# Kernel optimization log

Hardware: AMD Instinct MI355X
Metric: run time of the kernel (lower is better)

The kernel has to match this reference:

```python
import jax, jax.numpy as jnp
import numpy as np

WINDOW = (6, 7, 7)  # (agent_size, window_size, window_size)
HEADS = 8           # dim // dim_head = 256 // 32


def _relative_position_index(ws):
    d, h, w = ws
    coords = np.stack(np.meshgrid(np.arange(d), np.arange(h), np.arange(w), indexing='ij'))
    cf = coords.reshape(3, -1)                      # [3, n]
    rel = cf[:, :, None] - cf[:, None, :]           # [3, n, n]
    rel = rel.transpose(1, 2, 0).copy()             # [n, n, 3]
    rel[..., 0] += d - 1
    rel[..., 1] += h - 1
    rel[..., 2] += w - 1
    rel[..., 0] *= (2 * h - 1) * (2 * w - 1)
    rel[..., 1] *= (2 * w - 1)
    return rel.sum(-1)                              # [n, n] int

REL_IDX = jnp.asarray(_relative_position_index(WINDOW))


def setup_inputs() -> dict:
    key = jax.random.key(0)
    ks = jax.random.split(key, 7)
    dim = 256
    n_bias = (2 * WINDOW[0] - 1) * (2 * WINDOW[1] - 1) * (2 * WINDOW[2] - 1)  # 1859
    s = 0.02
    return {
        'x': jax.random.normal(ks[0], (2, 6, 12, 12, 7, 7, dim), jnp.float32),
        'Wq': jax.random.normal(ks[1], (dim, dim), jnp.float32) * s,
        'bq': jax.random.normal(ks[2], (dim,), jnp.float32) * s,
        'Wkv': jax.random.normal(ks[3], (dim, 2 * dim), jnp.float32) * s,
        'bkv': jax.random.normal(ks[4], (2 * dim,), jnp.float32) * s,
        'Wout': jax.random.normal(ks[5], (dim, dim), jnp.float32) * s,
        'bias_table': jax.random.normal(ks[6], (n_bias, HEADS), jnp.float32) * s,
    }


def reference(x, Wq, bq, Wkv, bkv, Wout, bias_table):
    b, l, gx, gy, w1, w2, d = x.shape
    h = HEADS
    dh = d // h
    n = l * w1 * w2
    B = b * gx * gy
    # 'b l x y w1 w2 d -> (b x y) (l w1 w2) d'  (agent-major token order)
    xt = jnp.transpose(x, (0, 2, 3, 1, 4, 5, 6)).reshape(B, n, d)
    q = xt @ Wq + bq                                  # [B, n, d]
    kv = xt @ Wkv + bkv                               # [B, n, 2d]
    k, v = kv[..., :d], kv[..., d:]
    split = lambda t: t.reshape(B, n, h, dh).transpose(0, 2, 1, 3)  # [B, h, n, dh]
    q, k, v = split(q), split(k), split(v)
    scale = dh ** -0.5
    sim = jnp.einsum('bhid,bhjd->bhij', q * scale, k)  # [B, h, n, n]
    bias = bias_table[REL_IDX]                         # [n, n, h]
    sim = sim + jnp.transpose(bias, (2, 0, 1))[None]
    attn = jax.nn.softmax(sim, axis=-1)
    out = jnp.einsum('bhij,bhjd->bhid', attn, v)       # [B, h, n, dh]
    out = out.transpose(0, 2, 1, 3).reshape(B, n, d) @ Wout
    # '(b x y) (l w1 w2) d -> b l x y w1 w2 d'
    out = out.reshape(b, gx, gy, l, w1, w2, d)
    return jnp.transpose(out, (0, 3, 1, 2, 4, 5, 6))
```

## Files before the change

### kernel.cpp

```cpp
#include <hip/hip_runtime.h>

#define DIM    256
#define NWIN   294
#define BWIN   288
#define MROWS  (BWIN * NWIN)
#define MPAD   84736
#define NHEADS 8
#define DH     32
#define NBIAS  1859

typedef __attribute__((ext_vector_type(8))) short  short8;
typedef __attribute__((ext_vector_type(4))) float  f32x4;

__device__ __forceinline__ unsigned short f2bf(float f) {
    unsigned int u = __float_as_uint(f);
    u += 0x7FFFu + ((u >> 16) & 1u);
    return (unsigned short)(u >> 16);
}

__device__ __forceinline__ void gl_lds16(const void* g, void* l) {
    __builtin_amdgcn_global_load_lds((const __attribute__((address_space(1))) unsigned int*)g,
                                     (__attribute__((address_space(3))) unsigned int*)l,
                                     16, 0, 0);
}

__global__ __launch_bounds__(256) void prep_x(const float* __restrict__ x,
                                              unsigned short* __restrict__ Xb)
{
    const int g   = blockIdx.x * 256 + threadIdx.x;
    const int row = g >> 5;
    const int col = (g & 31) * 8;
    if (row >= MPAD) return;
    uint4 pk;
    if (row < MROWS) {
        const int bw = row / NWIN, rw = row - bw * NWIN;
        const int bb = bw / 144,  r2 = bw - bb * 144;
        const int gxi = r2 / 12,  gyi = r2 - gxi * 12;
        const int lz = rw / 49,   r3 = rw - lz * 49;
        const int wa = r3 / 7,    wb = r3 - wa * 7;
        const float* src = x + ((((((size_t)bb * 6 + lz) * 12 + gxi) * 12 + gyi) * 7 + wa) * 7 + wb) * DIM + col;
        const float4 f0 = *(const float4*)(src);
        const float4 f1 = *(const float4*)(src + 4);
        pk.x = (unsigned)f2bf(f0.x) | ((unsigned)f2bf(f0.y) << 16);
        pk.y = (unsigned)f2bf(f0.z) | ((unsigned)f2bf(f0.w) << 16);
        pk.z = (unsigned)f2bf(f1.x) | ((unsigned)f2bf(f1.y) << 16);
        pk.w = (unsigned)f2bf(f1.z) | ((unsigned)f2bf(f1.w) << 16);
    } else {
        pk = (uint4){0u, 0u, 0u, 0u};
    }
    *(uint4*)(Xb + (size_t)row * 256 + col) = pk;
}

__global__ __launch_bounds__(256) void prep_w(const float* __restrict__ Wq,
                                              const float* __restrict__ Wkv,
                                              const float* __restrict__ Wout,
                                              unsigned short* __restrict__ Wt,
                                              unsigned short* __restrict__ Wot)
{
    const int g = blockIdx.x * 256 + threadIdx.x;
    if (g < 768 * 256) {
        const int n = g >> 8, k = g & 255;
        const float v = (n < 256) ? Wq[k * 256 + n] : Wkv[k * 512 + (n - 256)];
        Wt[g] = f2bf(v);
    } else {
        const int g2 = g - 768 * 256;
        const int n = g2 >> 8, k = g2 & 255;
        Wot[g2] = f2bf(Wout[k * 256 + n]);
    }
}

__global__ __launch_bounds__(256) void gemm_qkv(
    const unsigned short* __restrict__ Xb, const unsigned short* __restrict__ Wt,
    const float* __restrict__ bq, const float* __restrict__ bkv,
    unsigned short* __restrict__ Qb, unsigned short* __restrict__ Kb,
    unsigned short* __restrict__ Vtb)
{
    __shared__ __align__(16) unsigned short As[128 * 64];
    __shared__ __align__(16) unsigned short Bs[128 * 64];

    const int bn = blockIdx.x % 6;
    const int bm = blockIdx.x / 6;
    const int tileM = bm * 128;
    const int tileN = bn * 128;

    const int t    = threadIdx.x;
    const int w    = t >> 6;
    const int lane = t & 63;
    const int quad = lane >> 4;
    const int l15  = lane & 15;
    const int wm   = w >> 1, wn = w & 1;

    const int rA = lane >> 3;
    const int kA = (lane & 7) * 8;
    const unsigned short* aBase = Xb + ((size_t)tileM + rA) * 256 + kA;
    const unsigned short* bBase = Wt + ((size_t)tileN + rA) * 256 + kA;

    f32x4 acc[4][4] = {};

    for (int kb = 0; kb < 4; ++kb) {
        const int k0 = kb * 64;
        __syncthreads();
#pragma unroll
        for (int i = 0; i < 4; ++i) {
            const int c = w * 4 + i;
            gl_lds16(aBase + (size_t)c * 8 * 256 + k0, &As[c * 512]);
            gl_lds16(bBase + (size_t)c * 8 * 256 + k0, &Bs[c * 512]);
        }
        __syncthreads();
#pragma unroll
        for (int c2 = 0; c2 < 2; ++c2) {
            const int kk = c2 * 32 + quad * 8;
            short8 a[4], b[4];
#pragma unroll
            for (int mi = 0; mi < 4; ++mi)
                a[mi] = *(const short8*)&As[(wm * 64 + mi * 16 + l15) * 64 + kk];
#pragma unroll
            for (int ni = 0; ni < 4; ++ni)
                b[ni] = *(const short8*)&Bs[(wn * 64 + ni * 16 + l15) * 64 + kk];
#pragma unroll
            for (int mi = 0; mi < 4; ++mi)
#pragma unroll
                for (int ni = 0; ni < 4; ++ni)
                    acc[mi][ni] = __builtin_amdgcn_mfma_f32_16x16x32_bf16(a[mi], b[ni], acc[mi][ni], 0, 0, 0);
        }
    }

    const int colB = tileN + wn * 64;
    float bias[4];
#pragma unroll
    for (int ni = 0; ni < 4; ++ni) {
        const int n = colB + ni * 16 + l15;
        bias[ni] = (n < 256) ? bq[n] : bkv[n - 256];
    }
    const int rowB = tileM + wm * 64 + quad * 4;
#pragma unroll
    for (int mi = 0; mi < 4; ++mi) {
#pragma unroll
        for (int r = 0; r < 4; ++r) {
            const int row = rowB + mi * 16 + r;
            if (row < MROWS) {
                const int bw = row / NWIN;
                const int rw = row - bw * NWIN;
#pragma unroll
                for (int ni = 0; ni < 4; ++ni) {
                    const int n = colB + ni * 16 + l15;
                    const unsigned short v = f2bf(acc[mi][ni][r] + bias[ni]);
                    const int ch = n & 255;
                    const int hd = ch >> 5, di = ch & 31;
                    if (n < 512) {
                        unsigned short* dst = (n < 256) ? Qb : Kb;
                        dst[((size_t)(bw * NHEADS + hd) * NWIN + rw) * DH + di] = v;
                    } else {
                        Vtb[((size_t)(bw * NHEADS + hd) * DH + di) * NWIN + rw] = v;
                    }
                }
            }
        }
    }
}

__global__ __launch_bounds__(256, 3) void attn_kernel(
    const unsigned short* __restrict__ Qb, const unsigned short* __restrict__ Kb,
    const unsigned short* __restrict__ Vtb, const float* __restrict__ bias_table,
    unsigned short* __restrict__ Ob)
{
    const int bh   = blockIdx.x;
    const int bwin = bh >> 3;
    const int h    = bh & 7;

    __shared__ __align__(16) unsigned short Ks[304 * 32];
    __shared__ __align__(16) unsigned short Vts[32 * 328];
    __shared__ __align__(16) unsigned short Pc[4 * 16 * 32];
    __shared__ float          biasH[NBIAS];
    __shared__ unsigned short cIdx[304];

    const int t    = threadIdx.x;
    const int w    = t >> 6;
    const int lane = t & 63;
    const int quad = lane >> 4;
    const int l15  = lane & 15;

    {
        const uint4* Kg4 = (const uint4*)(Kb + (size_t)bh * (NWIN * DH));
        for (int i = t; i < (NWIN * DH) / 8; i += 256) ((uint4*)Ks)[i] = Kg4[i];
        for (int i = NWIN * DH + t; i < 304 * 32; i += 256) Ks[i] = 0;
    }
    {
        const unsigned short* Vg = Vtb + (size_t)bh * (DH * NWIN);
        for (int i = t; i < 32 * 328; i += 256) {
            const int r = i / 328, c = i - r * 328;
            Vts[i] = (c < NWIN) ? Vg[r * NWIN + c] : (unsigned short)0;
        }
    }
    for (int i = t; i < NBIAS; i += 256) biasH[i] = bias_table[i * NHEADS + h];
    for (int i = t; i < 304; i += 256) {
        if (i < NWIN) {
            const int l = i / 49, r = i - l * 49;
            cIdx[i] = (unsigned short)(169 * l + 13 * (r / 7) + (r - (r / 7) * 7));
        } else cIdx[i] = 0;
    }
    __syncthreads();

    const float scale = 0.17677669529663687f;
    const unsigned short* Qg = Qb + (size_t)bh * (NWIN * DH);
    unsigned short* Pw = Pc + w * (16 * 32);

#pragma unroll
    for (int r5 = 0; r5 < 5; ++r5) {
        const int it = 4 * r5 + w;
        if (it < 19) {
            short8 qf;
            const int qrow = it * 16 + l15;
            if (qrow < NWIN) qf = *(const short8*)(Qg + qrow * DH + quad * 8);
            else             qf = (short8){0,0,0,0,0,0,0,0};

            f32x4 S[19];
#pragma unroll
            for (int jt = 0; jt < 19; ++jt) {
                const short8 bf = *(const short8*)(Ks + (jt * 16 + l15) * 32 + quad * 8);
                S[jt] = __builtin_amdgcn_mfma_f32_16x16x32_bf16(qf, bf, (f32x4){0.f,0.f,0.f,0.f}, 0, 0, 0);
            }

            int cj[19];
#pragma unroll
            for (int jt = 0; jt < 19; ++jt) cj[jt] = cIdx[jt * 16 + l15];

            const int rowb = it * 16 + quad * 4;
            float inv[4];
#pragma unroll
            for (int r = 0; r < 4; ++r) {
                const int ci = (int)cIdx[rowb + r] + 929;
                float m = -1e30f;
#pragma unroll
                for (int jt = 0; jt < 19; ++jt) {
                    float s = S[jt][r] * scale + biasH[ci - cj[jt]];
                    if (jt == 18 && l15 >= 6) s = -1e30f;
                    S[jt][r] = s;
                    m = fmaxf(m, s);
                }
                m = fmaxf(m, __shfl_xor(m, 1));
                m = fmaxf(m, __shfl_xor(m, 2));
                m = fmaxf(m, __shfl_xor(m, 4));
                m = fmaxf(m, __shfl_xor(m, 8));
                float lsum = 0.f;
#pragma unroll
                for (int jt = 0; jt < 19; ++jt) {
                    const float p = __expf(S[jt][r] - m);
                    S[jt][r] = p;
                    lsum += p;
                }
                lsum += __shfl_xor(lsum, 1);
                lsum += __shfl_xor(lsum, 2);
                lsum += __shfl_xor(lsum, 4);
                lsum += __shfl_xor(lsum, 8);
                inv[r] = 1.0f / lsum;
            }

            f32x4 o0 = {0.f,0.f,0.f,0.f}, o1 = {0.f,0.f,0.f,0.f};
#pragma unroll
            for (int kt = 0; kt < 10; ++kt) {
                const int jt0 = 2 * kt, jt1 = 2 * kt + 1;
#pragma unroll
                for (int r = 0; r < 4; ++r) {
                    Pw[(quad * 4 + r) * 32 + l15]      = f2bf(S[jt0][r]);
                    Pw[(quad * 4 + r) * 32 + 16 + l15] = (jt1 < 19) ? f2bf(S[jt1][r]) : (unsigned short)0;
                }
                __asm__ volatile("s_waitcnt lgkmcnt(0)" ::: "memory");
                const short8 pa = *(const short8*)(Pw + l15 * 32 + quad * 8);
                const short8 v0 = *(const short8*)(Vts + l15 * 328 + kt * 32 + quad * 8);
                const short8 v1 = *(const short8*)(Vts + (16 + l15) * 328 + kt * 32 + quad * 8);
                o0 = __builtin_amdgcn_mfma_f32_16x16x32_bf16(pa, v0, o0, 0, 0, 0);
                o1 = __builtin_amdgcn_mfma_f32_16x16x32_bf16(pa, v1, o1, 0, 0, 0);
                __asm__ volatile("s_waitcnt lgkmcnt(0)" ::: "memory");
            }

#pragma unroll
            for (int r = 0; r < 4; ++r) {
                const int rg = it * 16 + quad * 4 + r;
                if (rg < NWIN) {
                    unsigned short* op = Ob + ((size_t)bwin * NWIN + rg) * DIM + h * DH;
                    op[l15]      = f2bf(o0[r] * inv[r]);
                    op[16 + l15] = f2bf(o1[r] * inv[r]);
                }
            }
        }
    }
}

__global__ __launch_bounds__(256) void gemm_out(
    const unsigned short* __restrict__ Ob, const unsigned short* __restrict__ Wot,
    float* __restrict__ out)
{
    __shared__ __align__(16) unsigned short As[128 * 64];
    __shared__ __align__(16) unsigned short Bs[128 * 64];

    const int bn = blockIdx.x & 1;
    const int bm = blockIdx.x >> 1;
    const int tileM = bm * 128;
    const int tileN = bn * 128;

    const int t    = threadIdx.x;
    const int w    = t >> 6;
    const int lane = t & 63;
    const int quad = lane >> 4;
    const int l15  = lane & 15;
    const int wm   = w >> 1, wn = w & 1;

    const int rA = lane >> 3;
    const int kA = (lane & 7) * 8;
    const unsigned short* aBase = Ob  + ((size_t)tileM + rA) * 256 + kA;
    const unsigned short* bBase = Wot + ((size_t)tileN + rA) * 256 + kA;

    f32x4 acc[4][4] = {};

    for (int kb = 0; kb < 4; ++kb) {
        const int k0 = kb * 64;
        __syncthreads();
#pragma unroll
        for (int i = 0; i < 4; ++i) {
            const int c = w * 4 + i;
            gl_lds16(aBase + (size_t)c * 8 * 256 + k0, &As[c * 512]);
            gl_lds16(bBase + (size_t)c * 8 * 256 + k0, &Bs[c * 512]);
        }
        __syncthreads();
#pragma unroll
        for (int c2 = 0; c2 < 2; ++c2) {
            const int kk = c2 * 32 + quad * 8;
            short8 a[4], b[4];
#pragma unroll
            for (int mi = 0; mi < 4; ++mi)
                a[mi] = *(const short8*)&As[(wm * 64 + mi * 16 + l15) * 64 + kk];
#pragma unroll
            for (int ni = 0; ni < 4; ++ni)
                b[ni] = *(const short8*)&Bs[(wn * 64 + ni * 16 + l15) * 64 + kk];
#pragma unroll
            for (int mi = 0; mi < 4; ++mi)
#pragma unroll
                for (int ni = 0; ni < 4; ++ni)
                    acc[mi][ni] = __builtin_amdgcn_mfma_f32_16x16x32_bf16(a[mi], b[ni], acc[mi][ni], 0, 0, 0);
        }
    }

    const int colB = tileN + wn * 64;
    const int rowB = tileM + wm * 64 + quad * 4;
#pragma unroll
    for (int mi = 0; mi < 4; ++mi) {
#pragma unroll
        for (int r = 0; r < 4; ++r) {
            const int row = rowB + mi * 16 + r;
            if (row < MROWS) {
                const int bw = row / NWIN, rw = row - bw * NWIN;
                const int bb = bw / 144,  r2 = bw - bb * 144;
                const int gxi = r2 / 12,  gyi = r2 - gxi * 12;
                const int lz = rw / 49,   r3 = rw - lz * 49;
                const int wa = r3 / 7,    wb = r3 - wa * 7;
                float* orow = out + ((((((size_t)bb * 6 + lz) * 12 + gxi) * 12 + gyi) * 7 + wa) * 7 + wb) * DIM;
#pragma unroll
                for (int ni = 0; ni < 4; ++ni)
                    orow[colB + ni * 16 + l15] = acc[mi][ni][r];
            }
        }
    }
}

extern "C" void kernel_launch(void* const* d_in, const int* in_sizes, int n_in,
                              void* d_out, int out_size, void* d_ws, size_t ws_size,
                              hipStream_t stream)
{
    const float* x          = (const float*)d_in[0];
    const float* Wq         = (const float*)d_in[1];
    const float* bq         = (const float*)d_in[2];
    const float* Wkv        = (const float*)d_in[3];
    const float* bkv        = (const float*)d_in[4];
    const float* Wout       = (const float*)d_in[5];
    const float* bias_table = (const float*)d_in[6];
    float* out = (float*)d_out;

    const size_t planePad = (size_t)MPAD * DIM;
    const size_t plane    = (size_t)MROWS * DIM;
    unsigned short* Xb  = (unsigned short*)d_ws;
    unsigned short* Qb  = Xb + planePad;
    unsigned short* Kb  = Qb + plane;
    unsigned short* Vtb = Kb + plane;
    unsigned short* Ob  = Vtb + plane;
    unsigned short* Wt  = Ob + planePad;
    unsigned short* Wot = Wt + 768 * 256;

    prep_x<<<MPAD / 8, 256, 0, stream>>>(x, Xb);
    prep_w<<<1024, 256, 0, stream>>>(Wq, Wkv, Wout, Wt, Wot);
    gemm_qkv<<<662 * 6, 256, 0, stream>>>(Xb, Wt, bq, bkv, Qb, Kb, Vtb);
    attn_kernel<<<BWIN * NHEADS, 256, 0, stream>>>(Qb, Kb, Vtb, bias_table, Ob);
    gemm_out<<<662 * 2, 256, 0, stream>>>(Ob, Wot, out);
}
```

Measured before the change: 443.8 us.

## Restructure attention softmax: transposed QK, no max, register P shuffle, MFMA row sums

```diff
diff --git a/kernel.cpp b/kernel.cpp
--- a/kernel.cpp
+++ b/kernel.cpp
@@ -1,4 +1,5 @@
 #include <hip/hip_runtime.h>
+#include <hip/hip_bf16.h>
 
 #define DIM    256
 #define NWIN   294
@@ -16,6 +17,13 @@
     unsigned int u = __float_as_uint(f);
     u += 0x7FFFu + ((u >> 16) & 1u);
     return (unsigned short)(u >> 16);
+}
+
+__device__ __forceinline__ unsigned pk2bf(float a, float b) {
+    __hip_bfloat162 h = __float22bfloat162_rn(float2{a, b});
+    unsigned u;
+    __builtin_memcpy(&u, &h, 4);
+    return u;
 }
 
 __device__ __forceinline__ void gl_lds16(const void* g, void* l) {
@@ -41,10 +49,10 @@
         const float* src = x + ((((((size_t)bb * 6 + lz) * 12 + gxi) * 12 + gyi) * 7 + wa) * 7 + wb) * DIM + col;
         const float4 f0 = *(const float4*)(src);
         const float4 f1 = *(const float4*)(src + 4);
-        pk.x = (unsigned)f2bf(f0.x) | ((unsigned)f2bf(f0.y) << 16);
-        pk.y = (unsigned)f2bf(f0.z) | ((unsigned)f2bf(f0.w) << 16);
-        pk.z = (unsigned)f2bf(f1.x) | ((unsigned)f2bf(f1.y) << 16);
-        pk.w = (unsigned)f2bf(f1.z) | ((unsigned)f2bf(f1.w) << 16);
+        pk.x = pk2bf(f0.x, f0.y);
+        pk.y = pk2bf(f0.z, f0.w);
+        pk.z = pk2bf(f1.x, f1.y);
+        pk.w = pk2bf(f1.z, f1.w);
     } else {
         pk = (uint4){0u, 0u, 0u, 0u};
     }
@@ -168,11 +176,10 @@
     const int bwin = bh >> 3;
     const int h    = bh & 7;
 
-    __shared__ __align__(16) unsigned short Ks[304 * 32];
+    __shared__ __align__(16) unsigned short Ks[304 * 40];
     __shared__ __align__(16) unsigned short Vts[32 * 328];
-    __shared__ __align__(16) unsigned short Pc[4 * 16 * 32];
-    __shared__ float          biasH[NBIAS];
-    __shared__ unsigned short cIdx[304];
+    __shared__ float          biasHs[NBIAS];
+    __shared__ __align__(8) unsigned short cIdx[304];
 
     const int t    = threadIdx.x;
     const int w    = t >> 6;
@@ -181,9 +188,13 @@
     const int l15  = lane & 15;
 
     {
-        const uint4* Kg4 = (const uint4*)(Kb + (size_t)bh * (NWIN * DH));
-        for (int i = t; i < (NWIN * DH) / 8; i += 256) ((uint4*)Ks)[i] = Kg4[i];
-        for (int i = NWIN * DH + t; i < 304 * 32; i += 256) Ks[i] = 0;
+        const unsigned short* Kg = Kb + (size_t)bh * (NWIN * DH);
+        for (int i = t; i < 304 * 4; i += 256) {
+            const int row = i >> 2, seg = i & 3;
+            uint4 v = (uint4){0u, 0u, 0u, 0u};
+            if (row < NWIN) v = *(const uint4*)(Kg + row * 32 + seg * 8);
+            *(uint4*)(Ks + row * 40 + seg * 8) = v;
+        }
     }
     {
         const unsigned short* Vg = Vtb + (size_t)bh * (DH * NWIN);
@@ -192,7 +203,7 @@
             Vts[i] = (c < NWIN) ? Vg[r * NWIN + c] : (unsigned short)0;
         }
     }
-    for (int i = t; i < NBIAS; i += 256) biasH[i] = bias_table[i * NHEADS + h];
+    for (int i = t; i < NBIAS; i += 256) biasHs[i] = bias_table[i * NHEADS + h] * 1.44269504088896f;
     for (int i = t; i < 304; i += 256) {
         if (i < NWIN) {
             const int l = i / 49, r = i - l * 49;
@@ -201,9 +212,11 @@
     }
     __syncthreads();
 
-    const float scale = 0.17677669529663687f;
+    const float SL2E = 0.25503486f;
     const unsigned short* Qg = Qb + (size_t)bh * (NWIN * DH);
-    unsigned short* Pw = Pc + w * (16 * 32);
+    const int   srcB = ((quad & 1) << 5) + l15;
+    const bool  hiSel = (quad >= 2);
+    const short8 ones = (short8){0x3F80,0x3F80,0x3F80,0x3F80,0x3F80,0x3F80,0x3F80,0x3F80};
 
 #pragma unroll
     for (int r5 = 0; r5 < 5; ++r5) {
@@ -214,73 +227,70 @@
             if (qrow < NWIN) qf = *(const short8*)(Qg + qrow * DH + quad * 8);
             else             qf = (short8){0,0,0,0,0,0,0,0};
 
+            const int ciB = (int)cIdx[it * 16 + l15] + 929;
+            const float* bbase = biasHs + ciB;
+
             f32x4 S[19];
 #pragma unroll
             for (int jt = 0; jt < 19; ++jt) {
-                const short8 bf = *(const short8*)(Ks + (jt * 16 + l15) * 32 + quad * 8);
-                S[jt] = __builtin_amdgcn_mfma_f32_16x16x32_bf16(qf, bf, (f32x4){0.f,0.f,0.f,0.f}, 0, 0, 0);
-            }
-
-            int cj[19];
-#pragma unroll
-            for (int jt = 0; jt < 19; ++jt) cj[jt] = cIdx[jt * 16 + l15];
-
-            const int rowb = it * 16 + quad * 4;
-            float inv[4];
-#pragma unroll
-            for (int r = 0; r < 4; ++r) {
-                const int ci = (int)cIdx[rowb + r] + 929;
-                float m = -1e30f;
-#pragma unroll
-                for (int jt = 0; jt < 19; ++jt) {
-                    float s = S[jt][r] * scale + biasH[ci - cj[jt]];
-                    if (jt == 18 && l15 >= 6) s = -1e30f;
-                    S[jt][r] = s;
-                    m = fmaxf(m, s);
+                const short8 kf = *(const short8*)(Ks + (jt * 16 + l15) * 40 + quad * 8);
+                S[jt] = __builtin_amdgcn_mfma_f32_16x16x32_bf16(kf, qf, (f32x4){0.f,0.f,0.f,0.f}, 0, 0, 0);
+            }
+
+            unsigned pk0[20], pk1[20];
+            pk0[19] = 0u; pk1[19] = 0u;
+#pragma unroll
+            for (int jt = 0; jt < 19; ++jt) {
+                const ushort4 c4 = *(const ushort4*)(cIdx + jt * 16 + quad * 4);
+                float p0 = exp2f(fmaf(S[jt][0], SL2E, bbase[-(int)c4.x]));
+                float p1 = exp2f(fmaf(S[jt][1], SL2E, bbase[-(int)c4.y]));
+                float p2 = exp2f(fmaf(S[jt][2], SL2E, bbase[-(int)c4.z]));
+                float p3 = exp2f(fmaf(S[jt][3], SL2E, bbase[-(int)c4.w]));
+                if (jt == 18) {
+                    if (quad * 4 + 0 >= 6) p0 = 0.f;
+                    if (quad * 4 + 1 >= 6) p1 = 0.f;
+                    if (quad * 4 + 2 >= 6) p2 = 0.f;
+                    if (quad * 4 + 3 >= 6) p3 = 0.f;
                 }
-                m = fmaxf(m, __shfl_xor(m, 1));
-                m = fmaxf(m, __shfl_xor(m, 2));
-                m = fmaxf(m, __shfl_xor(m, 4));
-                m = fmaxf(m, __shfl_xor(m, 8));
-                float lsum = 0.f;
-#pragma unroll
-                for (int jt = 0; jt < 19; ++jt) {
-                    const float p = __expf(S[jt][r] - m);
-                    S[jt][r] = p;
-                    lsum += p;
-                }
-                lsum += __shfl_xor(lsum, 1);
-                lsum += __shfl_xor(lsum, 2);
-                lsum += __shfl_xor(lsum, 4);
-                lsum += __shfl_xor(lsum, 8);
-                inv[r] = 1.0f / lsum;
-            }
-
-            f32x4 o0 = {0.f,0.f,0.f,0.f}, o1 = {0.f,0.f,0.f,0.f};
+                pk0[jt] = pk2bf(p0, p1);
+                pk1[jt] = pk2bf(p2, p3);
+            }
+
+            f32x4 o0 = {0.f,0.f,0.f,0.f}, o1 = {0.f,0.f,0.f,0.f}, o2 = {0.f,0.f,0.f,0.f};
 #pragma unroll
             for (int kt = 0; kt < 10; ++kt) {
-                const int jt0 = 2 * kt, jt1 = 2 * kt + 1;
-#pragma unroll
-                for (int r = 0; r < 4; ++r) {
-                    Pw[(quad * 4 + r) * 32 + l15]      = f2bf(S[jt0][r]);
-                    Pw[(quad * 4 + r) * 32 + 16 + l15] = (jt1 < 19) ? f2bf(S[jt1][r]) : (unsigned short)0;
-                }
-                __asm__ volatile("s_waitcnt lgkmcnt(0)" ::: "memory");
-                const short8 pa = *(const short8*)(Pw + l15 * 32 + quad * 8);
+                const int e0 = (int)pk0[2 * kt], e1 = (int)pk0[2 * kt + 1];
+                const int f0 = (int)pk1[2 * kt], f1 = (int)pk1[2 * kt + 1];
+                const unsigned aLo = (unsigned)__shfl(e0, srcB);
+                const unsigned aHi = (unsigned)__shfl(e1, srcB);
+                const unsigned bLo = (unsigned)__shfl(f0, srcB);
+                const unsigned bHi = (unsigned)__shfl(f1, srcB);
+                const unsigned cLo = (unsigned)__shfl(e0, srcB + 16);
+                const unsigned cHi = (unsigned)__shfl(e1, srcB + 16);
+                const unsigned dLo = (unsigned)__shfl(f0, srcB + 16);
+                const unsigned dHi = (unsigned)__shfl(f1, srcB + 16);
+                uint4 pw;
+                pw.x = hiSel ? aHi : aLo;
+                pw.y = hiSel ? bHi : bLo;
+                pw.z = hiSel ? cHi : cLo;
+                pw.w = hiSel ? dHi : dLo;
+                short8 pa;
+                __builtin_memcpy(&pa, &pw, 16);
                 const short8 v0 = *(const short8*)(Vts + l15 * 328 + kt * 32 + quad * 8);
                 const short8 v1 = *(const short8*)(Vts + (16 + l15) * 328 + kt * 32 + quad * 8);
                 o0 = __builtin_amdgcn_mfma_f32_16x16x32_bf16(pa, v0, o0, 0, 0, 0);
                 o1 = __builtin_amdgcn_mfma_f32_16x16x32_bf16(pa, v1, o1, 0, 0, 0);
-                __asm__ volatile("s_waitcnt lgkmcnt(0)" ::: "memory");
+                o2 = __builtin_amdgcn_mfma_f32_16x16x32_bf16(pa, ones, o2, 0, 0, 0);
             }
 
 #pragma unroll
             for (int r = 0; r < 4; ++r) {
                 const int rg = it * 16 + quad * 4 + r;
                 if (rg < NWIN) {
+                    const float inv = 1.0f / o2[r];
                     unsigned short* op = Ob + ((size_t)bwin * NWIN + rg) * DIM + h * DH;
-                    op[l15]      = f2bf(o0[r] * inv[r]);
-                    op[16 + l15] = f2bf(o1[r] * inv[r]);
+                    op[l15]      = f2bf(o0[r] * inv);
+                    op[16 + l15] = f2bf(o1[r] * inv);
                 }
             }
         }
```

After: 438.0 us. Within noise of the previous version (-1.3%).
